# Performance work log

Measured on AMD Instinct MI355X. Metric: run time of the kernel, lower is better.

Reference implementation:

```python
import jax, jax.numpy as jnp
import numpy as np
import math


def setup_inputs() -> dict:
    key = jax.random.key(0)
    k1, k2 = jax.random.split(key)
    x = jax.random.normal(k1, (8, 256, 56, 56), dtype=jnp.float32)
    w = jax.random.normal(k2, (8, 32, 9, 56, 56), dtype=jnp.float32)
    return {"x": x, "w": w}


def _unfold(x, K):
    # x: (B, C, H, W) -> (B, C, K*K, H, W) patches (same padding, stride 1)
    B, C, H, W = x.shape
    pad = (K - 1) // 2
    xp = jnp.pad(x, ((0, 0), (0, 0), (pad, pad), (pad, pad)))
    patches = [xp[:, :, i:i + H, j:j + W] for i in range(K) for j in range(K)]
    return jnp.stack(patches, axis=2)


def reference(x, w):
    B, C, H, W = x.shape
    G, K2 = w.shape[1], w.shape[2]
    K = int(math.isqrt(K2))
    cpg = C // G  # channels per group; torch repeat tiles so channel c uses group c % G
    xu = _unfold(x, K)  # (B, C, K2, H, W)
    xu = xu.reshape(B, cpg, G, K2, H, W)
    out = jnp.einsum('bigkhw,bgkhw->bighw', xu, w)  # sum over K2
    return out.reshape(B, C, H, W)
```

## Files before the change

kernel.cpp:

```cpp
#include <hip/hip_runtime.h>


#define B_DIM 8
#define C_DIM 256
#define G_DIM 32
#define CPG 8
#define H_DIM 56
#define W_DIM 56
#define HW 3136
#define SLICES 7

__global__ __launch_bounds__(256) void SKA_20950850470021_kernel(
    const float* __restrict__ x, const float* __restrict__ wt,
    float* __restrict__ out) {
  const int bg = blockIdx.x;
  const int b  = bg >> 5;
  const int g  = bg & 31;

  const float* wbase = wt + (size_t)bg * 9 * HW;
  const float* xbase = x  + ((size_t)b * C_DIM + g) * HW;
  float*       obase = out + ((size_t)b * C_DIM + g) * HW;

  const int p0 = blockIdx.y * 448;
  for (int p = p0 + threadIdx.x; p < p0 + 448; p += 256) {
    const int h  = p / W_DIM;
    const int wp = p - h * W_DIM;

    float wk[9];
#pragma unroll
    for (int k = 0; k < 9; ++k) wk[k] = wbase[(size_t)k * HW + p];

#pragma unroll
    for (int i = 0; i < CPG; ++i) {
      const float* xc = xbase + (size_t)(i * G_DIM) * HW;
      float acc = 0.f;
#pragma unroll
      for (int di = 0; di < 3; ++di) {
        const int hh = h + di - 1;
        const bool hok = (unsigned)hh < (unsigned)H_DIM;
#pragma unroll
        for (int dj = 0; dj < 3; ++dj) {
          const int ww = wp + dj - 1;
          const bool ok = hok && ((unsigned)ww < (unsigned)W_DIM);
          const float xv = ok ? xc[hh * W_DIM + ww] : 0.f;
          acc = fmaf(xv, wk[di * 3 + dj], acc);
        }
      }
      obase[(size_t)(i * G_DIM) * HW + p] = acc;
    }
  }
}

extern "C" void kernel_launch(void* const* d_in, const int* in_sizes, int n_in,
                              void* d_out, int out_size, void* d_ws, size_t ws_size,
                              hipStream_t stream) {
  const float* x  = (const float*)d_in[0];
  const float* wt = (const float*)d_in[1];
  float* out = (float*)d_out;

  dim3 grid(B_DIM * G_DIM, SLICES);
  SKA_20950850470021_kernel<<<grid, 256, 0, stream>>>(x, wt, out);
}
```

Measured before the change: 102.3 us.

## Register-tile 2x4 output pixels per thread with vectorized loads and masked weights

Each thread now computes a 2-row by 4-column output tile for four channels of a group, loading the weights as float4 once and reusing a 4x6 register window of x across the 3x3 taps. Boundary handling moves from per-load predicates to zeroed weights and clamped indices. The grid is flattened to 784 blocks with channels split into two halves per group. The intent is fewer scalar loads and branches and better bandwidth through 128-bit accesses, at the cost of more registers per thread and less weight reuse across channels per thread.

```diff
diff --git a/kernel.cpp b/kernel.cpp
--- a/kernel.cpp
+++ b/kernel.cpp
@@ -1,53 +1,100 @@
 #include <hip/hip_runtime.h>
 
 
-#define B_DIM 8
-#define C_DIM 256
-#define G_DIM 32
-#define CPG 8
+#define W_DIM 56
 #define H_DIM 56
-#define W_DIM 56
 #define HW 3136
-#define SLICES 7
 
 __global__ __launch_bounds__(256) void SKA_20950850470021_kernel(
     const float* __restrict__ x, const float* __restrict__ wt,
     float* __restrict__ out) {
-  const int bg = blockIdx.x;
-  const int b  = bg >> 5;
-  const int g  = bg & 31;
+  const int t  = blockIdx.x * 256 + threadIdx.x;
+  const int ct = t % 14;
+  const int t2 = t / 14;
+  const int rp = t2 % 28;
+  const int t3 = t2 / 28;
+  const int i0 = t3 & 1;
+  const int pg = t3 >> 1;
+  const int b  = pg >> 5;
+  const int g  = pg & 31;
 
-  const float* wbase = wt + (size_t)bg * 9 * HW;
-  const float* xbase = x  + ((size_t)b * C_DIM + g) * HW;
-  float*       obase = out + ((size_t)b * C_DIM + g) * HW;
+  const int wp = ct * 4;
+  const int h0 = rp * 2;
 
-  const int p0 = blockIdx.y * 448;
-  for (int p = p0 + threadIdx.x; p < p0 + 448; p += 256) {
-    const int h  = p / W_DIM;
-    const int wp = p - h * W_DIM;
+  const float* wbase = wt + (size_t)pg * 9 * HW + h0 * W_DIM + wp;
+  float4 wk[2][9];
+#pragma unroll
+  for (int k = 0; k < 9; ++k) {
+    wk[0][k] = *(const float4*)(wbase + (size_t)k * HW);
+    wk[1][k] = *(const float4*)(wbase + (size_t)k * HW + W_DIM);
+  }
 
-    float wk[9];
+  const float mtop = (h0 == 0) ? 0.f : 1.f;
+  const float mbot = (h0 == 54) ? 0.f : 1.f;
 #pragma unroll
-    for (int k = 0; k < 9; ++k) wk[k] = wbase[(size_t)k * HW + p];
+  for (int k = 0; k < 3; ++k) {
+    wk[0][k].x *= mtop; wk[0][k].y *= mtop; wk[0][k].z *= mtop; wk[0][k].w *= mtop;
+    wk[1][k + 6].x *= mbot; wk[1][k + 6].y *= mbot; wk[1][k + 6].z *= mbot; wk[1][k + 6].w *= mbot;
+  }
+  const float mleft = (wp == 0) ? 0.f : 1.f;
+  const float mright = (wp == 52) ? 0.f : 1.f;
+#pragma unroll
+  for (int d = 0; d < 2; ++d)
+#pragma unroll
+    for (int di = 0; di < 3; ++di) {
+      wk[d][di * 3 + 0].x *= mleft;
+      wk[d][di * 3 + 2].w *= mright;
+    }
 
+  int rh[4];
 #pragma unroll
-    for (int i = 0; i < CPG; ++i) {
-      const float* xc = xbase + (size_t)(i * G_DIM) * HW;
-      float acc = 0.f;
+  for (int r = 0; r < 4; ++r) {
+    int hh = h0 - 1 + r;
+    hh = hh < 0 ? 0 : (hh > 55 ? 55 : hh);
+    rh[r] = hh * W_DIM;
+  }
+  const int cs0 = (wp == 0) ? 0 : wp - 1;
+  const int cs5 = (wp == 52) ? 55 : wp + 4;
+
+  const float* xplane = x + ((size_t)b * 256 + (size_t)i0 * 4 * 32 + g) * HW;
+  float*       oplane = out + ((size_t)b * 256 + (size_t)i0 * 4 * 32 + g) * HW;
+  const int    opix   = h0 * W_DIM + wp;
+
+#pragma unroll 2
+  for (int j = 0; j < 4; ++j) {
+    const float* xc = xplane + (size_t)(j * 32) * HW;
+
+    float xr[4][6];
 #pragma unroll
-      for (int di = 0; di < 3; ++di) {
-        const int hh = h + di - 1;
-        const bool hok = (unsigned)hh < (unsigned)H_DIM;
+    for (int r = 0; r < 4; ++r) {
+      const float* rowp = xc + rh[r];
+      xr[r][0] = rowp[cs0];
+      const float4 m = *(const float4*)(rowp + wp);
+      xr[r][1] = m.x; xr[r][2] = m.y; xr[r][3] = m.z; xr[r][4] = m.w;
+      xr[r][5] = rowp[cs5];
+    }
+
+    float4 a0 = make_float4(0.f, 0.f, 0.f, 0.f);
+    float4 a1 = make_float4(0.f, 0.f, 0.f, 0.f);
 #pragma unroll
-        for (int dj = 0; dj < 3; ++dj) {
-          const int ww = wp + dj - 1;
-          const bool ok = hok && ((unsigned)ww < (unsigned)W_DIM);
-          const float xv = ok ? xc[hh * W_DIM + ww] : 0.f;
-          acc = fmaf(xv, wk[di * 3 + dj], acc);
-        }
+    for (int di = 0; di < 3; ++di)
+#pragma unroll
+      for (int dj = 0; dj < 3; ++dj) {
+        const float4 W0 = wk[0][di * 3 + dj];
+        const float4 W1 = wk[1][di * 3 + dj];
+        a0.x = fmaf(xr[di][dj + 0], W0.x, a0.x);
+        a0.y = fmaf(xr[di][dj + 1], W0.y, a0.y);
+        a0.z = fmaf(xr[di][dj + 2], W0.z, a0.z);
+        a0.w = fmaf(xr[di][dj + 3], W0.w, a0.w);
+        a1.x = fmaf(xr[di + 1][dj + 0], W1.x, a1.x);
+        a1.y = fmaf(xr[di + 1][dj + 1], W1.y, a1.y);
+        a1.z = fmaf(xr[di + 1][dj + 2], W1.z, a1.z);
+        a1.w = fmaf(xr[di + 1][dj + 3], W1.w, a1.w);
       }
-      obase[(size_t)(i * G_DIM) * HW + p] = acc;
-    }
+
+    float* op = oplane + (size_t)(j * 32) * HW + opix;
+    *(float4*)op = a0;
+    *(float4*)(op + W_DIM) = a1;
   }
 }
 
@@ -58,6 +105,5 @@
   const float* wt = (const float*)d_in[1];
   float* out = (float*)d_out;
 
-  dim3 grid(B_DIM * G_DIM, SLICES);
-  SKA_20950850470021_kernel<<<grid, 256, 0, stream>>>(x, wt, out);
+  SKA_20950850470021_kernel<<<dim3(784), dim3(256), 0, stream>>>(x, wt, out);
 }
```

After: 106.1 us. 1.04x slower.

## Stage input bands in LDS and compute four outputs per thread with vector loads

Applied to the files above, without the earlier changes.

Each block loads a 14-row band (plus halo) of the 8 channels sharing a group into shared memory with zero-padded columns, then each thread computes a 4-wide output strip using float4 weight loads and float4 stores. This replaces scattered, bounds-checked scalar global loads with coalesced vector loads and LDS reuse across the 3x3 neighborhood. About a quarter of threads sit idle in the compute phase, and the grid shrinks to 1024 blocks.

```diff
diff --git a/kernel.cpp b/kernel.cpp
--- a/kernel.cpp
+++ b/kernel.cpp
@@ -1,53 +1,85 @@
 #include <hip/hip_runtime.h>
 
 
-#define B_DIM 8
-#define C_DIM 256
-#define G_DIM 32
-#define CPG 8
-#define H_DIM 56
+#define HW 3136
 #define W_DIM 56
-#define HW 3136
-#define SLICES 7
+#define LDS_STRIDE 60
+#define BAND 14
+#define XROWS 16
 
 __global__ __launch_bounds__(256) void SKA_20950850470021_kernel(
     const float* __restrict__ x, const float* __restrict__ wt,
     float* __restrict__ out) {
-  const int bg = blockIdx.x;
-  const int b  = bg >> 5;
-  const int g  = bg & 31;
+  __shared__ float lx[8 * XROWS * LDS_STRIDE];
 
-  const float* wbase = wt + (size_t)bg * 9 * HW;
-  const float* xbase = x  + ((size_t)b * C_DIM + g) * HW;
-  float*       obase = out + ((size_t)b * C_DIM + g) * HW;
+  const int pg   = blockIdx.x;
+  const int band = blockIdx.y;
+  const int h0   = band * BAND;
+  const int b    = pg >> 5;
+  const int g    = pg & 31;
+  const int tid  = threadIdx.x;
 
-  const int p0 = blockIdx.y * 448;
-  for (int p = p0 + threadIdx.x; p < p0 + 448; p += 256) {
-    const int h  = p / W_DIM;
-    const int wp = p - h * W_DIM;
+  {
+    const int ch  = tid >> 5;
+    const int r   = (tid >> 1) & 15;
+    const int col = (tid & 1) ? 57 : 0;
+    lx[(ch * XROWS + r) * LDS_STRIDE + col] = 0.f;
+  }
 
-    float wk[9];
+  const float* xg = x + ((size_t)b * 256 + g) * HW;
+  for (int it = 0; it < 7; ++it) {
+    const int idx = tid + it * 256;
+    const int j   = idx % 14;
+    const int u   = idx / 14;
+    const int ch  = u >> 4;
+    const int r   = u & 15;
+    const int gr  = h0 + r - 1;
+    float4 v = make_float4(0.f, 0.f, 0.f, 0.f);
+    if ((unsigned)gr < 56u)
+      v = *(const float4*)(xg + (size_t)ch * 32 * HW + gr * W_DIM + 4 * j);
+    float* d = &lx[(ch * XROWS + r) * LDS_STRIDE + 1 + 4 * j];
+    d[0] = v.x; d[1] = v.y; d[2] = v.z; d[3] = v.w;
+  }
+
+  __syncthreads();
+
+  if (tid >= BAND * 14) return;
+  const int q  = tid % 14;
+  const int r  = tid / 14;
+  const int gr = h0 + r;
+  const int c0 = 4 * q;
+
+  const float* wb = wt + (size_t)pg * 9 * HW + gr * W_DIM + c0;
+  float4 wk[9];
 #pragma unroll
-    for (int k = 0; k < 9; ++k) wk[k] = wbase[(size_t)k * HW + p];
+  for (int k = 0; k < 9; ++k) wk[k] = *(const float4*)(wb + (size_t)k * HW);
+
+  float* ob = out + ((size_t)b * 256 + g) * HW + gr * W_DIM + c0;
 
 #pragma unroll
-    for (int i = 0; i < CPG; ++i) {
-      const float* xc = xbase + (size_t)(i * G_DIM) * HW;
-      float acc = 0.f;
+  for (int ch = 0; ch < 8; ++ch) {
+    float xr[3][6];
 #pragma unroll
-      for (int di = 0; di < 3; ++di) {
-        const int hh = h + di - 1;
-        const bool hok = (unsigned)hh < (unsigned)H_DIM;
+    for (int dr = 0; dr < 3; ++dr) {
+      const float* p = &lx[(ch * XROWS + r + dr) * LDS_STRIDE + 4 * q];
+      const float4 a = *(const float4*)p;
+      const float2 bb = *(const float2*)(p + 4);
+      xr[dr][0] = a.x; xr[dr][1] = a.y; xr[dr][2] = a.z; xr[dr][3] = a.w;
+      xr[dr][4] = bb.x; xr[dr][5] = bb.y;
+    }
+
+    float4 acc = make_float4(0.f, 0.f, 0.f, 0.f);
 #pragma unroll
-        for (int dj = 0; dj < 3; ++dj) {
-          const int ww = wp + dj - 1;
-          const bool ok = hok && ((unsigned)ww < (unsigned)W_DIM);
-          const float xv = ok ? xc[hh * W_DIM + ww] : 0.f;
-          acc = fmaf(xv, wk[di * 3 + dj], acc);
-        }
+    for (int di = 0; di < 3; ++di)
+#pragma unroll
+      for (int dj = 0; dj < 3; ++dj) {
+        const float4 W = wk[di * 3 + dj];
+        acc.x = fmaf(xr[di][dj + 0], W.x, acc.x);
+        acc.y = fmaf(xr[di][dj + 1], W.y, acc.y);
+        acc.z = fmaf(xr[di][dj + 2], W.z, acc.z);
+        acc.w = fmaf(xr[di][dj + 3], W.w, acc.w);
       }
-      obase[(size_t)(i * G_DIM) * HW + p] = acc;
-    }
+    *(float4*)(ob + (size_t)ch * 32 * HW) = acc;
   }
 }
 
@@ -58,6 +90,6 @@
   const float* wt = (const float*)d_in[1];
   float* out = (float*)d_out;
 
-  dim3 grid(B_DIM * G_DIM, SLICES);
+  dim3 grid(256, 4);
   SKA_20950850470021_kernel<<<grid, 256, 0, stream>>>(x, wt, out);
 }
```

Result: faster. 98.00 us (-4.2%).
